# Performance work log

Measured on AMD Instinct MI355X. Metric: run time of the kernel, lower is better.

The kernel has to match this reference:

```python
import jax, jax.numpy as jnp
import numpy as np

NUM_HEADS = 32
ROPE_BASE = 10000.0


def _rotate_half(x):
    h = x.shape[-1] // 2
    return jnp.concatenate([-x[..., h:], x[..., :h]], axis=-1)


def setup_inputs() -> dict:
    key = jax.random.key(0)
    ks = jax.random.split(key, 6)
    B, S, H = 2, 2048, 4096
    hidden_states = jax.random.normal(ks[0], (B, S, H), dtype=jnp.float32)
    # additive causal mask: 0 on/below diagonal, large negative above
    causal = jnp.tril(jnp.ones((S, S), dtype=bool))
    attention_mask = jnp.where(causal, 0.0, -1e9).astype(jnp.float32)
    attention_mask = jnp.broadcast_to(attention_mask[None, None], (B, 1, S, S))
    position_ids = jnp.broadcast_to(jnp.arange(S, dtype=jnp.int64 if jax.config.jax_enable_x64 else jnp.int32)[None, :], (B, S))
    scale = 1.0 / np.sqrt(H)
    Wq = jax.random.normal(ks[1], (H, H), dtype=jnp.float32) * scale
    Wk = jax.random.normal(ks[2], (H, H), dtype=jnp.float32) * scale
    Wv = jax.random.normal(ks[3], (H, H), dtype=jnp.float32) * scale
    Wo = jax.random.normal(ks[4], (H, H), dtype=jnp.float32) * scale
    return {"hidden_states": hidden_states, "attention_mask": attention_mask,
            "position_ids": position_ids, "Wq": Wq, "Wk": Wk, "Wv": Wv, "Wo": Wo}


def reference(hidden_states, attention_mask, position_ids, Wq, Wk, Wv, Wo):
    B, S, H = hidden_states.shape
    nh = NUM_HEADS
    hd = H // nh
    # QKV projections (torch Linear: y = x @ W.T), split heads -> [B, nh, S, hd]
    def proj(W):
        y = jnp.einsum('bsh,oh->bso', hidden_states, W)
        return y.reshape(B, S, nh, hd).transpose(0, 2, 1, 3)
    q, k, v = proj(Wq), proj(Wk), proj(Wv)
    # rotary embeddings gathered at position_ids
    inv_freq = 1.0 / (ROPE_BASE ** (jnp.arange(0, hd, 2, dtype=jnp.float32) / hd))
    freqs = position_ids.astype(jnp.float32)[:, :, None] * inv_freq[None, None, :]  # [B,S,hd/2]
    emb = jnp.concatenate([freqs, freqs], axis=-1)  # [B,S,hd]
    cos = jnp.cos(emb)[:, None, :, :]  # [B,1,S,hd]
    sin = jnp.sin(emb)[:, None, :, :]
    q = q * cos + _rotate_half(q) * sin
    k = k * cos + _rotate_half(k) * sin
    # scaled dot-product attention
    scores = jnp.einsum('bhqd,bhkd->bhqk', q, k) / jnp.sqrt(jnp.float32(hd))
    scores = scores + attention_mask
    scores = jnp.maximum(scores, jnp.finfo(scores.dtype).min)
    attn = jax.nn.softmax(scores, axis=-1)
    out = jnp.einsum('bhqk,bhkd->bhqd', attn, v)  # [B,nh,S,hd]
    out = out.transpose(0, 2, 1, 3).reshape(B, S, H)
    return jnp.einsum('bsh,oh->bso', out, Wo)
```

## Files before the change

### kernel.cpp

```cpp
#include <hip/hip_runtime.h>
#include <cstdint>
#include <cmath>

typedef __bf16 bf16;
typedef __bf16 bf16x8 __attribute__((ext_vector_type(8)));
typedef __bf16 bf16x4 __attribute__((ext_vector_type(4)));
typedef float f32x4 __attribute__((ext_vector_type(4)));

#define B_ 2
#define S_ 2048
#define H_ 4096
#define NH 32
#define HD 128

#define VMCNT(n) asm volatile("s_waitcnt vmcnt(" #n ")" ::: "memory")
#define BAR() __builtin_amdgcn_s_barrier()

__device__ __forceinline__ void gl_lds16(const void* g, void* l) {
  __builtin_amdgcn_global_load_lds(
      (const __attribute__((address_space(1))) unsigned int*)g,
      (__attribute__((address_space(3))) unsigned int*)l, 16, 0, 0);
}

__global__ __launch_bounds__(256) void cast_kernel(const float* __restrict__ in,
                                                   bf16* __restrict__ out, int n4) {
  int i = blockIdx.x * 256 + threadIdx.x;
  if (i < n4) {
    float4 v = ((const float4*)in)[i];
    bf16x4 o = {(bf16)v.x, (bf16)v.y, (bf16)v.z, (bf16)v.w};
    ((bf16x4*)out)[i] = o;
  }
}

template <int TM, int TN>
__device__ __forceinline__ void mfma_q(f32x4 (&acc)[8][4], bf16x8 (&a)[4][2],
                                       bf16x8 (&b)[2][2]) {
  __builtin_amdgcn_s_setprio(1);
#pragma unroll
  for (int i = 0; i < 4; ++i)
#pragma unroll
    for (int j = 0; j < 2; ++j)
#pragma unroll
      for (int kf = 0; kf < 2; ++kf)
        acc[TM * 4 + i][TN * 2 + j] = __builtin_amdgcn_mfma_f32_16x16x32_bf16(
            a[i][kf], b[j][kf], acc[TM * 4 + i][TN * 2 + j], 0, 0, 0);
  __builtin_amdgcn_s_setprio(0);
}

template <int EPI>
__global__ __launch_bounds__(512, 2) void gemm256(const bf16* __restrict__ A,
                                                  const bf16* __restrict__ Bw,
                                                  void* __restrict__ Cout) {
  constexpr int K = 4096, N = 4096, KT = K / 64;
  __shared__ __attribute__((aligned(16))) char lds[131072];
  char* Al = lds;
  char* Bl = lds + 65536;
  int tid = threadIdx.x;
  int l = tid & 63, lr = l & 15, lg = l >> 4;
  int w = tid >> 6, wm = w >> 2, wn = w & 3;
  int bid = (int)blockIdx.x;
  int swb = (bid & 7) * 32 + (bid >> 3);
  int r0 = (swb >> 4) * 256, c0 = (swb & 15) * 256;
  const bf16* Ab = A + (size_t)r0 * K;
  const bf16* Bb = Bw + (size_t)c0 * K;

  int lr0 = tid >> 3;
  int cel = (((tid & 7) ^ ((tid >> 3) & 7)) << 3);

  auto stageA = [&](int buf, int mh, int k0) {
    char* dst = Al + buf * 32768 + mh * 16384 + tid * 16;
    int ra = mh * 64 + lr0;
    gl_lds16(Ab + (size_t)ra * K + k0 + cel, dst);
    gl_lds16(Ab + (size_t)(ra + 128) * K + k0 + cel, dst + 8192);
  };
  auto stageB = [&](int buf, int nh, int k0) {
    char* dst = Bl + buf * 32768 + nh * 16384 + tid * 16;
    int n0 = (lr0 >> 5) * 64 + nh * 32 + (lr0 & 31);
    gl_lds16(Bb + (size_t)n0 * K + k0 + cel, dst);
    gl_lds16(Bb + (size_t)(n0 + 128) * K + k0 + cel, dst + 8192);
  };

  int rsw = (lr & 7) << 4;
  auto ldA = [&](bf16x8 (&dst)[4][2], int buf, int mh) {
    char* base = Al + buf * 32768 + mh * 16384 + wm * 8192;
#pragma unroll
    for (int mfl = 0; mfl < 4; ++mfl)
#pragma unroll
      for (int kf = 0; kf < 2; ++kf)
        __builtin_memcpy(&dst[mfl][kf],
                         base + (mfl * 16 + lr) * 128 + ((kf * 64 + lg * 16) ^ rsw), 16);
  };
  auto ldB = [&](bf16x8 (&dst)[2][2], int buf, int nh) {
    char* base = Bl + buf * 32768 + nh * 16384 + wn * 4096;
#pragma unroll
    for (int nfl = 0; nfl < 2; ++nfl)
#pragma unroll
      for (int kf = 0; kf < 2; ++kf)
        __builtin_memcpy(&dst[nfl][kf],
                         base + (nfl * 16 + lr) * 128 + ((kf * 64 + lg * 16) ^ rsw), 16);
  };

  bf16x8 af[4][2], bf0[2][2], bf1[2][2];
  f32x4 acc[8][4] = {};

  stageA(0, 0, 0);
  stageB(0, 0, 0);
  stageB(0, 1, 0);
  stageA(0, 1, 0);

  for (int kt = 0; kt < KT - 1; ++kt) {
    int buf = kt & 1, nb = buf ^ 1;
    int k0n = (kt + 1) * 64;
    VMCNT(2); BAR();
    ldA(af, buf, 0);
    ldB(bf0, buf, 0);
    stageA(nb, 0, k0n);
    mfma_q<0, 0>(acc, af, bf0);
    ldB(bf1, buf, 1);
    VMCNT(2);
    BAR();
    stageB(nb, 0, k0n);
    mfma_q<0, 1>(acc, af, bf1);
    ldA(af, buf, 1);
    BAR();
    stageB(nb, 1, k0n);
    mfma_q<1, 1>(acc, af, bf1);
    BAR();
    stageA(nb, 1, k0n);
    mfma_q<1, 0>(acc, af, bf0);
  }
  {
    int buf = (KT - 1) & 1;
    VMCNT(2); BAR();
    ldA(af, buf, 0);
    ldB(bf0, buf, 0);
    mfma_q<0, 0>(acc, af, bf0);
    ldB(bf1, buf, 1);
    VMCNT(0);
    BAR();
    mfma_q<0, 1>(acc, af, bf1);
    ldA(af, buf, 1);
    BAR();
    mfma_q<1, 1>(acc, af, bf1);
    mfma_q<1, 0>(acc, af, bf0);
  }

#pragma unroll
  for (int mf = 0; mf < 8; ++mf)
#pragma unroll
    for (int nf = 0; nf < 4; ++nf) {
      int orow = r0 + wm * 128 + mf * 16 + lg * 4;
      int ocol = c0 + wn * 64 + nf * 16 + lr;
      if (EPI == 0) {
        bf16* C = (bf16*)Cout;
#pragma unroll
        for (int jr = 0; jr < 4; ++jr)
          C[(size_t)(orow + jr) * N + ocol] = (bf16)acc[mf][nf][jr];
      } else {
        float* C = (float*)Cout;
#pragma unroll
        for (int jr = 0; jr < 4; ++jr)
          C[(size_t)(orow + jr) * N + ocol] = acc[mf][nf][jr];
      }
    }
}

__global__ __launch_bounds__(256) void rope_kernel(bf16* __restrict__ Qx,
                                                   bf16* __restrict__ Kx,
                                                   const int* __restrict__ pos,
                                                   float qscale) {
  int r = blockIdx.x;
  bf16* X = blockIdx.y ? Kx : Qx;
  float scale = blockIdx.y ? 1.0f : qscale;
  float pf = (float)pos[r];
  int i = threadIdx.x & 63;
  int h0 = threadIdx.x >> 6;
  float ang = pf * exp2f(-0.20762050593046868f * (float)i);
  float sn = sinf(ang), cs = cosf(ang);
  bf16* row = X + (size_t)r * H_;
#pragma unroll
  for (int h = h0; h < NH; h += 4) {
    bf16* p = row + h * HD + i;
    float a = (float)p[0], b = (float)p[64];
    p[0] = (bf16)((a * cs - b * sn) * scale);
    p[64] = (bf16)((b * cs + a * sn) * scale);
  }
}

__global__ __launch_bounds__(256) void transpose_v(const bf16* __restrict__ V,
                                                   bf16* __restrict__ Vt) {
  __shared__ __attribute__((aligned(16))) bf16 tile[64][130];
  int bh = blockIdx.y;
  int b = bh >> 5, h = bh & 31;
  int s0 = blockIdx.x * 64;
  int t = threadIdx.x;
  const bf16* src = V + (size_t)(b * S_ + s0) * H_ + h * HD;
  int rr = t >> 4, cc = (t & 15) * 8;
#pragma unroll
  for (int k = 0; k < 4; ++k) {
    bf16x8 v;
    __builtin_memcpy(&v, src + (size_t)(rr + k * 16) * H_ + cc, 16);
#pragma unroll
    for (int u = 0; u < 8; ++u) tile[rr + k * 16][cc + u] = v[u];
  }
  __syncthreads();
  bf16* dst = Vt + (size_t)bh * HD * S_;
  int sl = t & 63, d0 = t >> 6;
  for (int j = 0; j < 32; ++j) {
    int d = d0 + j * 4;
    dst[(size_t)d * S_ + s0 + sl] = tile[sl][d];
  }
}

__global__ __launch_bounds__(512, 4) void attn_kernel(const bf16* __restrict__ Q,
                                                      const bf16* __restrict__ Km,
                                                      const bf16* __restrict__ Vt,
                                                      bf16* __restrict__ Out) {
  __shared__ __attribute__((aligned(16))) bf16 Ks[2][64 * 128];
  __shared__ __attribute__((aligned(16))) bf16 Vs[2][128 * 64];
  __shared__ __attribute__((aligned(16))) bf16 P_lds[8][16 * 64];
  int tid = threadIdx.x;
  int w = tid >> 6, l = tid & 63;
  int lr = l & 15, lg = l >> 4;
  int bh = blockIdx.y, b = bh >> 5, h = bh & 31;
  int qt = 15 - (int)blockIdx.x;
  int q0w = qt * 128 + w * 16;
  const bf16* Qb = Q + (size_t)b * S_ * H_ + h * HD;
  const char* Kg = (const char*)(Km + (size_t)b * S_ * H_ + h * HD);
  const char* Vg = (const char*)(Vt + (size_t)bh * HD * S_);
  bf16* Ob = Out + (size_t)b * S_ * H_ + h * HD;

  bf16x8 qf[4];
#pragma unroll
  for (int dk = 0; dk < 4; ++dk)
    __builtin_memcpy(&qf[dk], Qb + (size_t)(q0w + lr) * H_ + dk * 32 + lg * 8, 16);

  f32x4 o[8] = {};
  float m = -INFINITY, ls = 0.f;
  int nkv_blk = 2 * qt + 2;
  int nkv_w = 2 * qt + (w >> 2) + 1;

  auto stageK = [&](int buf, int kv0) {
#pragma unroll
    for (int p = 0; p < 2; ++p) {
      int row = p * 32 + (tid >> 4);
      int src = ((tid & 15) * 16) ^ ((row & 7) << 4);
      gl_lds16(Kg + (size_t)(kv0 + row) * (H_ * 2) + src,
               (char*)&Ks[buf][0] + p * 8192 + w * 1024);
    }
  };
  auto stageV = [&](int buf, int kv0) {
#pragma unroll
    for (int p = 0; p < 2; ++p) {
      int row = p * 64 + (tid >> 3);
      int src = ((tid & 7) * 16) ^ ((row & 7) << 4);
      gl_lds16(Vg + (size_t)row * (S_ * 2) + (size_t)kv0 * 2 + src,
               (char*)&Vs[buf][0] + p * 8192 + w * 1024);
    }
  };

  stageK(0, 0);
  stageV(0, 0);
  __syncthreads();

  int cur = 0;
  char* Pl = (char*)&P_lds[w][0];
  for (int t = 0; t < nkv_blk; ++t) {
    int kv0 = t * 64;
    if (t + 1 < nkv_blk) {
      stageK(cur ^ 1, kv0 + 64);
      stageV(cur ^ 1, kv0 + 64);
    }
    if (t < nkv_w) {
      const char* Kl = (const char*)&Ks[cur][0];
      const char* Vl = (const char*)&Vs[cur][0];
      f32x4 s4[4] = {};
      __builtin_amdgcn_s_setprio(1);
#pragma unroll
      for (int dk = 0; dk < 4; ++dk)
#pragma unroll
        for (int st = 0; st < 4; ++st) {
          int row = st * 16 + lr;
          int cb = (dk * 64 + lg * 16) ^ ((row & 7) << 4);
          bf16x8 kf;
          __builtin_memcpy(&kf, Kl + row * 256 + cb, 16);
          s4[st] = __builtin_amdgcn_mfma_f32_16x16x32_bf16(kf, qf[dk], s4[st], 0, 0, 0);
        }
      __builtin_amdgcn_s_setprio(0);
      if (t == nkv_w - 1) {
        int qg = q0w + lr;
#pragma unroll
        for (int st = 0; st < 4; ++st)
#pragma unroll
          for (int j = 0; j < 4; ++j)
            if (kv0 + st * 16 + lg * 4 + j > qg) s4[st][j] = -INFINITY;
      }
      float mx = -INFINITY;
#pragma unroll
      for (int st = 0; st < 4; ++st)
#pragma unroll
        for (int j = 0; j < 4; ++j) mx = fmaxf(mx, s4[st][j]);
      mx = fmaxf(mx, __shfl_xor(mx, 16));
      mx = fmaxf(mx, __shfl_xor(mx, 32));
      float sc = 1.0f;
      if (!__all((int)(mx <= m + 8.0f))) {
        float mn = fmaxf(m, mx);
        sc = exp2f(m - mn);
        m = mn;
        float scq0 = __shfl(sc, lg * 4 + 0);
        float scq1 = __shfl(sc, lg * 4 + 1);
        float scq2 = __shfl(sc, lg * 4 + 2);
        float scq3 = __shfl(sc, lg * 4 + 3);
#pragma unroll
        for (int dt = 0; dt < 8; ++dt) {
          o[dt][0] *= scq0; o[dt][1] *= scq1; o[dt][2] *= scq2; o[dt][3] *= scq3;
        }
      }
      float pv[4][4], rs = 0.f;
#pragma unroll
      for (int st = 0; st < 4; ++st)
#pragma unroll
        for (int j = 0; j < 4; ++j) {
          pv[st][j] = exp2f(s4[st][j] - m);
          rs += pv[st][j];
        }
      rs += __shfl_xor(rs, 16);
      rs += __shfl_xor(rs, 32);
      ls = ls * sc + rs;
#pragma unroll
      for (int st = 0; st < 4; ++st) {
        bf16x4 pk = {(bf16)pv[st][0], (bf16)pv[st][1], (bf16)pv[st][2], (bf16)pv[st][3]};
        *(bf16x4*)(Pl + lr * 128 + ((st * 32 + lg * 8) ^ ((lr & 7) << 4))) = pk;
      }
      bf16x8 pa[2];
#pragma unroll
      for (int ks = 0; ks < 2; ++ks)
        __builtin_memcpy(&pa[ks], Pl + lr * 128 + ((ks * 64 + lg * 16) ^ ((lr & 7) << 4)), 16);
      __builtin_amdgcn_s_setprio(1);
#pragma unroll
      for (int dt = 0; dt < 8; ++dt)
#pragma unroll
        for (int ks = 0; ks < 2; ++ks) {
          int row = dt * 16 + lr;
          int cb = (ks * 64 + lg * 16) ^ ((row & 7) << 4);
          bf16x8 vf;
          __builtin_memcpy(&vf, Vl + row * 128 + cb, 16);
          o[dt] = __builtin_amdgcn_mfma_f32_16x16x32_bf16(pa[ks], vf, o[dt], 0, 0, 0);
        }
      __builtin_amdgcn_s_setprio(0);
    }
    __syncthreads();
    cur ^= 1;
  }
  float lsq[4];
#pragma unroll
  for (int j = 0; j < 4; ++j) lsq[j] = __shfl(ls, lg * 4 + j);
#pragma unroll
  for (int j = 0; j < 4; ++j) {
    float inv = 1.0f / lsq[j];
#pragma unroll
    for (int dt = 0; dt < 8; ++dt)
      Ob[(size_t)(q0w + lg * 4 + j) * H_ + dt * 16 + lr] = (bf16)(o[dt][j] * inv);
  }
}

extern "C" void kernel_launch(void* const* d_in, const int* in_sizes, int n_in,
                              void* d_out, int out_size, void* d_ws, size_t ws_size,
                              hipStream_t stream) {
  const float* X = (const float*)d_in[0];
  const int* pos = (const int*)d_in[2];
  const float* Wq = (const float*)d_in[3];
  const float* Wk = (const float*)d_in[4];
  const float* Wv = (const float*)d_in[5];
  const float* Wo = (const float*)d_in[6];
  float* out = (float*)d_out;
  char* ws = (char*)d_ws;
  const size_t MB32 = 32ull << 20;
  bf16* Xb = (bf16*)ws;
  bf16* Wb = (bf16*)(ws + MB32);
  bf16* Qb = (bf16*)(ws + 2 * MB32);
  bf16* Kb = (bf16*)(ws + 3 * MB32);
  bf16* Vb = (bf16*)(ws + 4 * MB32);
  bf16* Vt = (bf16*)(ws + 5 * MB32);

  const int n4 = (4096 * 4096) / 4;
  dim3 cgrid(n4 / 256), cblk(256);
  dim3 ggrid(256), gblk(512);

  cast_kernel<<<cgrid, cblk, 0, stream>>>(X, Xb, n4);
  cast_kernel<<<cgrid, cblk, 0, stream>>>(Wq, Wb, n4);
  gemm256<0><<<ggrid, gblk, 0, stream>>>(Xb, Wb, Qb);
  cast_kernel<<<cgrid, cblk, 0, stream>>>(Wk, Wb, n4);
  gemm256<0><<<ggrid, gblk, 0, stream>>>(Xb, Wb, Kb);
  cast_kernel<<<cgrid, cblk, 0, stream>>>(Wv, Wb, n4);
  gemm256<0><<<ggrid, gblk, 0, stream>>>(Xb, Wb, Vb);

  const float qscale = 1.4426950408889634f / 11.313708498984760f;
  rope_kernel<<<dim3(4096, 2), 256, 0, stream>>>(Qb, Kb, pos, qscale);
  transpose_v<<<dim3(32, 64), 256, 0, stream>>>(Vb, Vt);

  attn_kernel<<<dim3(16, 64), 512, 0, stream>>>(Qb, Kb, Vt, Xb);

  cast_kernel<<<cgrid, cblk, 0, stream>>>(Wo, Wb, n4);
  gemm256<1><<<ggrid, gblk, 0, stream>>>(Xb, Wb, out);
}
```

Measured before the change: 880.1 us.

## Process two query tiles per attention block to reuse staged K/V tiles

Each attention workgroup now handles 256 query rows, split into two 128-row sub-tiles per wave, instead of 128. Every K/V tile staged into LDS is consumed twice, which halves global K/V traffic and barrier count per query row. The grid shrinks to 8x64 blocks and launch bounds drop to 2 blocks per CU to allow the doubled register state. The trade-off is fewer blocks, lower occupancy and coarser causal load balancing.

```diff
diff --git a/kernel.cpp b/kernel.cpp
--- a/kernel.cpp
+++ b/kernel.cpp
@@ -212,7 +212,7 @@
   }
 }
 
-__global__ __launch_bounds__(512, 4) void attn_kernel(const bf16* __restrict__ Q,
+__global__ __launch_bounds__(512, 2) void attn_kernel(const bf16* __restrict__ Q,
                                                       const bf16* __restrict__ Km,
                                                       const bf16* __restrict__ Vt,
                                                       bf16* __restrict__ Out) {
@@ -223,22 +223,27 @@
   int w = tid >> 6, l = tid & 63;
   int lr = l & 15, lg = l >> 4;
   int bh = blockIdx.y, b = bh >> 5, h = bh & 31;
-  int qt = 15 - (int)blockIdx.x;
-  int q0w = qt * 128 + w * 16;
+  int qt = 7 - (int)blockIdx.x;
+  int q0a = qt * 256 + w * 16;
+  int q0b = q0a + 128;
   const bf16* Qb = Q + (size_t)b * S_ * H_ + h * HD;
   const char* Kg = (const char*)(Km + (size_t)b * S_ * H_ + h * HD);
   const char* Vg = (const char*)(Vt + (size_t)bh * HD * S_);
   bf16* Ob = Out + (size_t)b * S_ * H_ + h * HD;
 
-  bf16x8 qf[4];
-#pragma unroll
-  for (int dk = 0; dk < 4; ++dk)
-    __builtin_memcpy(&qf[dk], Qb + (size_t)(q0w + lr) * H_ + dk * 32 + lg * 8, 16);
-
-  f32x4 o[8] = {};
-  float m = -INFINITY, ls = 0.f;
-  int nkv_blk = 2 * qt + 2;
-  int nkv_w = 2 * qt + (w >> 2) + 1;
+  bf16x8 qfa[4], qfb[4];
+#pragma unroll
+  for (int dk = 0; dk < 4; ++dk) {
+    __builtin_memcpy(&qfa[dk], Qb + (size_t)(q0a + lr) * H_ + dk * 32 + lg * 8, 16);
+    __builtin_memcpy(&qfb[dk], Qb + (size_t)(q0b + lr) * H_ + dk * 32 + lg * 8, 16);
+  }
+
+  f32x4 oa[8] = {}, ob[8] = {};
+  float ma = -INFINITY, lsa = 0.f, mb = -INFINITY, lsb = 0.f;
+  int wq = w >> 2;
+  int nkv_blk = 4 * qt + 4;
+  int nkv_a = 4 * qt + 1 + wq;
+  int nkv_b = 4 * qt + 3 + wq;
 
   auto stageK = [&](int buf, int kv0) {
 #pragma unroll
@@ -271,9 +276,12 @@
       stageK(cur ^ 1, kv0 + 64);
       stageV(cur ^ 1, kv0 + 64);
     }
-    if (t < nkv_w) {
-      const char* Kl = (const char*)&Ks[cur][0];
-      const char* Vl = (const char*)&Vs[cur][0];
+    const char* Kl = (const char*)&Ks[cur][0];
+    const char* Vl = (const char*)&Vs[cur][0];
+
+    auto process = [&](bf16x8 (&qf)[4], f32x4 (&o)[8], float& m, float& ls,
+                       int nkv_w, int qg0) {
+      if (t >= nkv_w) return;
       f32x4 s4[4] = {};
       __builtin_amdgcn_s_setprio(1);
 #pragma unroll
@@ -288,7 +296,7 @@
         }
       __builtin_amdgcn_s_setprio(0);
       if (t == nkv_w - 1) {
-        int qg = q0w + lr;
+        int qg = qg0 + lr;
 #pragma unroll
         for (int st = 0; st < 4; ++st)
 #pragma unroll
@@ -348,19 +356,37 @@
           o[dt] = __builtin_amdgcn_mfma_f32_16x16x32_bf16(pa[ks], vf, o[dt], 0, 0, 0);
         }
       __builtin_amdgcn_s_setprio(0);
-    }
+    };
+
+    process(qfa, oa, ma, lsa, nkv_a, q0a);
+    process(qfb, ob, mb, lsb, nkv_b, q0b);
+
     __syncthreads();
     cur ^= 1;
   }
-  float lsq[4];
-#pragma unroll
-  for (int j = 0; j < 4; ++j) lsq[j] = __shfl(ls, lg * 4 + j);
-#pragma unroll
-  for (int j = 0; j < 4; ++j) {
-    float inv = 1.0f / lsq[j];
-#pragma unroll
-    for (int dt = 0; dt < 8; ++dt)
-      Ob[(size_t)(q0w + lg * 4 + j) * H_ + dt * 16 + lr] = (bf16)(o[dt][j] * inv);
+  {
+    float lsq[4];
+#pragma unroll
+    for (int j = 0; j < 4; ++j) lsq[j] = __shfl(lsa, lg * 4 + j);
+#pragma unroll
+    for (int j = 0; j < 4; ++j) {
+      float inv = 1.0f / lsq[j];
+#pragma unroll
+      for (int dt = 0; dt < 8; ++dt)
+        Ob[(size_t)(q0a + lg * 4 + j) * H_ + dt * 16 + lr] = (bf16)(oa[dt][j] * inv);
+    }
+  }
+  {
+    float lsq[4];
+#pragma unroll
+    for (int j = 0; j < 4; ++j) lsq[j] = __shfl(lsb, lg * 4 + j);
+#pragma unroll
+    for (int j = 0; j < 4; ++j) {
+      float inv = 1.0f / lsq[j];
+#pragma unroll
+      for (int dt = 0; dt < 8; ++dt)
+        Ob[(size_t)(q0b + lg * 4 + j) * H_ + dt * 16 + lr] = (bf16)(ob[dt][j] * inv);
+    }
   }
 }
 
@@ -399,7 +425,7 @@
   rope_kernel<<<dim3(4096, 2), 256, 0, stream>>>(Qb, Kb, pos, qscale);
   transpose_v<<<dim3(32, 64), 256, 0, stream>>>(Vb, Vt);
 
-  attn_kernel<<<dim3(16, 64), 512, 0, stream>>>(Qb, Kb, Vt, Xb);
+  attn_kernel<<<dim3(8, 64), 512, 0, stream>>>(Qb, Kb, Vt, Xb);
 
   cast_kernel<<<cgrid, cblk, 0, stream>>>(Wo, Wb, n4);
   gemm256<1><<<ggrid, gblk, 0, stream>>>(Xb, Wb, out);
```

Result: slower. 911.9 us (+3.6%).
